# Kernel optimization log

Measured on AMD Instinct MI355X. Metric: run time of the kernel, lower is better.

Reference implementation:

```python
import jax, jax.numpy as jnp
import numpy as np
from jax import lax

# Fixed-point format: Q*.8 (8 fractional bits), as used by HGRNFixed8bit's
# to_fixed/from_fixed round-trip. We simulate it in float via round(x*256)/256.
FRAC = 256.0
EPS = 1e-5
B, T, D = 4, 2048, 2048  # batch, seq_len, hidden_size; input_dim = D (expand_ratio=1)


def to_fixed(x):
    return jnp.round(x * FRAC) / FRAC


def to_ternary(w):
    # BitNet-style ternarization: sign(w/mean|w|), zeroed where |w_norm| < 0.5
    scale = jnp.mean(jnp.abs(w))
    wn = w / (scale + 1e-5)
    t = jnp.sign(wn)
    return jnp.where(jnp.abs(wn) < 0.5, 0.0, t).astype(jnp.float32)


def per_channel_scale(w):
    # compute_scale: mean |w| over dim 0, stored in fixed point
    return to_fixed(jnp.mean(jnp.abs(w), axis=0))


def setup_inputs() -> dict:
    key = jax.random.key(0)
    ks = jax.random.split(key, 6)
    hidden_states = jax.random.normal(ks[0], (B, T, D), dtype=jnp.float32)
    # float master weights, then quantize exactly as quantize_weights() does
    w_i_f = jax.random.normal(ks[1], (D, D), dtype=jnp.float32) * 0.02  # i_proj.weight.T
    w_f_f = jax.random.normal(ks[2], (D, D), dtype=jnp.float32) * 0.02  # f_proj.weight.T
    w_g_f = jax.random.normal(ks[3], (D, D), dtype=jnp.float32) * 0.02  # g_proj.weight.T
    w_o_f = jax.random.normal(ks[4], (D, D), dtype=jnp.float32) * 0.02  # o_proj.weight [D_out, D_in]
    g_norm_w = jnp.ones((D,), dtype=jnp.float32)  # g_norm (RMSNorm-swish-gate) weight
    return {
        "hidden_states": hidden_states,
        "w_i": to_ternary(w_i_f), "w_f": to_ternary(w_f_f),
        "w_g": to_ternary(w_g_f), "w_o": to_ternary(w_o_f),
        "s_i": per_channel_scale(w_i_f), "s_f": per_channel_scale(w_f_f),
        "s_g": per_channel_scale(w_g_f), "s_o": per_channel_scale(w_o_f),
        "g_norm_w": g_norm_w,
    }


def reference(hidden_states, w_i, w_f, w_g, w_o, s_i, s_f, s_g, s_o, g_norm_w):
    # Quantize activations to 8-bit fixed point (to_fixed)
    x = to_fixed(hidden_states)                       # [B,T,D]
    # Ternary dequant-matmuls with per-channel scales
    i = jnp.einsum('btd,de->bte', x, w_i) * s_i       # input branch
    f = jax.nn.sigmoid(jnp.einsum('btd,de->bte', x, w_f) * s_f)  # forget gate
    g = jnp.einsum('btd,de->bte', x, w_g) * s_g       # output gate
    i = (1.0 - f) * i                                 # HGRN input gating
    # Gated linear recurrence h_t = f_t * h_{t-1} + i_t via associative scan
    def combine(a, b):
        af, ai = a
        bf, bi = b
        return (af * bf, ai * bf + bi)
    _, h = lax.associative_scan(combine, (f, i), axis=1)  # [B,T,E]
    # FusedRMSNormSwishGate: rmsnorm(h) * weight * swish(g)
    rms = h * lax.rsqrt(jnp.mean(h * h, axis=-1, keepdims=True) + EPS)
    o = rms * g_norm_w * (g * jax.nn.sigmoid(g))
    # Output ternary matmul (o_proj, weight untransposed -> use w_o.T),
    # per-input-channel scale, then from_fixed round-trip of the fixed output
    out = to_fixed(jnp.einsum('bte,oe->bto', o * s_o, w_o))  # [B,T,D]
    return out
```

## Files before the change

kernel.cpp:

```cpp
#include <hip/hip_runtime.h>
#include <hip/hip_bf16.h>
#include <stdint.h>
#include <math.h>


#define BATCH 4
#define SEQ   2048
#define DIM   2048
#define MROWS (BATCH*SEQ)
#define TCH   64
#define NCH   (SEQ/TCH)

#define BM 128
#define BN 128
#define BK 32

typedef unsigned short u16;
typedef __attribute__((ext_vector_type(8))) short short8;
typedef __attribute__((ext_vector_type(4))) float f32x4;

static __device__ __forceinline__ u16 f2bf_rne(float x) {
  uint32_t u = __float_as_uint(x);
  u += 0x7FFFu + ((u >> 16) & 1u);
  return (u16)(u >> 16);
}
static __device__ __forceinline__ float bf2f(u16 h) {
  return __uint_as_float(((uint32_t)h) << 16);
}

static __device__ __forceinline__ void gl2lds16(const void* g, void* l) {
  __builtin_amdgcn_global_load_lds((const __attribute__((address_space(1))) void*)g,
                                   (__attribute__((address_space(3))) void*)l,
                                   16, 0, 0);
}

__global__ __launch_bounds__(256) void diag_ws(float* __restrict__ out, float val) {
  size_t i = ((size_t)blockIdx.x * 256 + threadIdx.x) * 8;
#pragma unroll
  for (int j = 0; j < 8; j++) out[i + j] = val;
}

__global__ __launch_bounds__(256) void prep_x(const float* __restrict__ x,
                                              u16* __restrict__ XB) {
  size_t i = ((size_t)blockIdx.x * 256 + threadIdx.x) * 4;
  float4 v = *(const float4*)(x + i);
  float q[4] = {v.x, v.y, v.z, v.w};
  u16 hh[4];
#pragma unroll
  for (int j = 0; j < 4; j++) {
    float xq = rintf(q[j] * 256.0f) * 0.00390625f;
    hh[j] = f2bf_rne(xq);
  }
  *(uint2*)(XB + i) = make_uint2((uint32_t)hh[0] | ((uint32_t)hh[1] << 16),
                                 (uint32_t)hh[2] | ((uint32_t)hh[3] << 16));
}

__global__ void prep_wT(const float* __restrict__ w_i, const float* __restrict__ w_f,
                        const float* __restrict__ w_g, u16* __restrict__ WT) {
  __shared__ u16 tile[32][33];
  const int g = blockIdx.z;
  const float* __restrict__ w = (g == 0) ? w_i : (g == 1) ? w_f : w_g;
  u16* __restrict__ outp = WT + (size_t)g * DIM * DIM;
  const int d0 = blockIdx.x * 32;
  const int e0 = blockIdx.y * 32;
  const int tx = threadIdx.x;
  const int ty = threadIdx.y;
  for (int ii = ty; ii < 32; ii += 8)
    tile[ii][tx] = f2bf_rne(w[(size_t)(d0 + ii) * DIM + e0 + tx]);
  __syncthreads();
  for (int ii = ty; ii < 32; ii += 8)
    outp[(size_t)(e0 + ii) * DIM + d0 + tx] = tile[tx][ii];
}

__global__ __launch_bounds__(256) void prep_wo(const float* __restrict__ w, u16* __restrict__ WB) {
  size_t i = ((size_t)blockIdx.x * 256 + threadIdx.x) * 4;
  float4 v = *(const float4*)(w + i);
  *(uint2*)(WB + i) = make_uint2((uint32_t)f2bf_rne(v.x) | ((uint32_t)f2bf_rne(v.y) << 16),
                                 (uint32_t)f2bf_rne(v.z) | ((uint32_t)f2bf_rne(v.w) << 16));
}

__global__ __launch_bounds__(256) void gemm_gates(
    const u16* __restrict__ XB, const u16* __restrict__ WT,
    const float* __restrict__ s_i, const float* __restrict__ s_f, const float* __restrict__ s_g,
    const float* __restrict__ gnw, const float* __restrict__ s_o,
    u16* __restrict__ Ib, u16* __restrict__ Fb, u16* __restrict__ Gb) {
  __shared__ u16 sA[BM * BK];
  __shared__ u16 sB[BN * BK];

  const int bid = blockIdx.x;
  const int xcd = bid & 7;
  const int i5 = bid >> 3;
  const int gate = i5 >> 7;
  const int r = i5 & 127;
  const int n0 = (r & 15) * BN;
  const int m0 = (xcd * 8 + (r >> 4)) * BM;

  const u16* __restrict__ Wg = WT + (size_t)gate * DIM * DIM;
  const int tid = threadIdx.x;
  const int lane16 = tid & 15;
  const int quad = (tid & 63) >> 4;
  const int waveM = (tid >> 6) >> 1;
  const int waveN = (tid >> 6) & 1;
  const int srow = tid >> 2;
  const int scol = (tid & 3) * 8;

  f32x4 acc[4][4];
#pragma unroll
  for (int a = 0; a < 4; a++)
#pragma unroll
    for (int b = 0; b < 4; b++) acc[a][b] = {0.f, 0.f, 0.f, 0.f};

  for (int k0 = 0; k0 < DIM; k0 += BK) {
    __syncthreads();
#pragma unroll
    for (int j = 0; j < 2; j++) {
      const int row = srow + j * 64;
      gl2lds16(XB + (size_t)(m0 + row) * DIM + k0 + scol, sA + row * BK + scol);
      gl2lds16(Wg + (size_t)(n0 + row) * DIM + k0 + scol, sB + row * BK + scol);
    }
    __syncthreads();

    short8 af[4], bf[4];
#pragma unroll
    for (int mi = 0; mi < 4; mi++)
      af[mi] = *(const short8*)(sA + (waveM * 64 + mi * 16 + lane16) * BK + quad * 8);
#pragma unroll
    for (int ni = 0; ni < 4; ni++)
      bf[ni] = *(const short8*)(sB + (waveN * 64 + ni * 16 + lane16) * BK + quad * 8);
#pragma unroll
    for (int mi = 0; mi < 4; mi++)
#pragma unroll
      for (int ni = 0; ni < 4; ni++)
        acc[mi][ni] = __builtin_amdgcn_mfma_f32_16x16x32_bf16(af[mi], bf[ni], acc[mi][ni], 0, 0, 0);
  }

  const float* __restrict__ sc = (gate == 0) ? s_i : (gate == 1) ? s_f : s_g;
  u16* __restrict__ Out = (gate == 0) ? Ib : (gate == 1) ? Fb : Gb;
#pragma unroll
  for (int ni = 0; ni < 4; ni++) {
    const int n = n0 + waveN * 64 + ni * 16 + lane16;
    const float scale = sc[n];
    const float post = (gate == 2) ? gnw[n] * s_o[n] : 0.f;
#pragma unroll
    for (int mi = 0; mi < 4; mi++) {
      const int mbase = m0 + waveM * 64 + mi * 16 + quad * 4;
#pragma unroll
      for (int r2 = 0; r2 < 4; r2++) {
        float v = acc[mi][ni][r2] * scale;
        if (gate == 1) v = 1.0f / (1.0f + expf(-v));
        if (gate == 2) v = v / (1.0f + expf(-v)) * post;
        Out[(size_t)(mbase + r2) * DIM + n] = f2bf_rne(v);
      }
    }
  }
}

__global__ __launch_bounds__(256) void scan_phase1(const u16* __restrict__ Fb,
                                                   const u16* __restrict__ Ib,
                                                   float* __restrict__ Pc,
                                                   float* __restrict__ Sc) {
  const int e0 = (blockIdx.x * 256 + threadIdx.x) * 2;
  const int c = blockIdx.y;
  const int b = blockIdx.z;
  const size_t base = ((size_t)b * SEQ + (size_t)c * TCH) * DIM + e0;
  float P0 = 1.f, S0 = 0.f, P1 = 1.f, S1 = 0.f;
  for (int t = 0; t < TCH; t++) {
    const uint32_t fp = *(const uint32_t*)(Fb + base + (size_t)t * DIM);
    const uint32_t ip = *(const uint32_t*)(Ib + base + (size_t)t * DIM);
    const float f0 = bf2f((u16)fp), f1 = bf2f((u16)(fp >> 16));
    const float i0 = bf2f((u16)ip), i1 = bf2f((u16)(ip >> 16));
    S0 = S0 * f0 + (1.f - f0) * i0;  P0 *= f0;
    S1 = S1 * f1 + (1.f - f1) * i1;  P1 *= f1;
  }
  const size_t ci = ((size_t)b * NCH + c) * DIM + e0;
  *(float2*)(Pc + ci) = make_float2(P0, P1);
  *(float2*)(Sc + ci) = make_float2(S0, S1);
}

__global__ __launch_bounds__(256) void scan_phase2(const u16* __restrict__ Fb,
                                                   const u16* __restrict__ Ib,
                                                   const float* __restrict__ Pc,
                                                   const float* __restrict__ Sc,
                                                   u16* __restrict__ Hb) {
  const int e0 = (blockIdx.x * 256 + threadIdx.x) * 2;
  const int c = blockIdx.y;
  const int b = blockIdx.z;
  float h0 = 0.f, h1 = 0.f;
  for (int cc = 0; cc < c; cc++) {
    const size_t ci = ((size_t)b * NCH + cc) * DIM + e0;
    const float2 p = *(const float2*)(Pc + ci);
    const float2 s = *(const float2*)(Sc + ci);
    h0 = s.x + p.x * h0;
    h1 = s.y + p.y * h1;
  }
  const size_t base = ((size_t)b * SEQ + (size_t)c * TCH) * DIM + e0;
  for (int t = 0; t < TCH; t++) {
    const uint32_t fp = *(const uint32_t*)(Fb + base + (size_t)t * DIM);
    const uint32_t ip = *(const uint32_t*)(Ib + base + (size_t)t * DIM);
    const float f0 = bf2f((u16)fp), f1 = bf2f((u16)(fp >> 16));
    const float i0 = bf2f((u16)ip), i1 = bf2f((u16)(ip >> 16));
    h0 = f0 * h0 + (1.f - f0) * i0;
    h1 = f1 * h1 + (1.f - f1) * i1;
    *(uint32_t*)(Hb + base + (size_t)t * DIM) =
        (uint32_t)f2bf_rne(h0) | ((uint32_t)f2bf_rne(h1) << 16);
  }
}

__global__ __launch_bounds__(256) void rms_gate(const u16* __restrict__ Hb,
                                                const u16* __restrict__ SwGb,
                                                u16* __restrict__ OS) {
  const size_t base = (size_t)blockIdx.x * DIM;
  const int tid = threadIdx.x;
  const int e0 = tid * 8;
  uint4 hp = *(const uint4*)(Hb + base + e0);
  float hv[8];
  hv[0] = bf2f((u16)hp.x); hv[1] = bf2f((u16)(hp.x >> 16));
  hv[2] = bf2f((u16)hp.y); hv[3] = bf2f((u16)(hp.y >> 16));
  hv[4] = bf2f((u16)hp.z); hv[5] = bf2f((u16)(hp.z >> 16));
  hv[6] = bf2f((u16)hp.w); hv[7] = bf2f((u16)(hp.w >> 16));
  float ss = 0.f;
#pragma unroll
  for (int j = 0; j < 8; j++) ss += hv[j] * hv[j];
#pragma unroll
  for (int off = 32; off > 0; off >>= 1) ss += __shfl_down(ss, off, 64);
  __shared__ float red[4];
  if ((tid & 63) == 0) red[tid >> 6] = ss;
  __syncthreads();
  const float tot = red[0] + red[1] + red[2] + red[3];
  const float inv = 1.0f / sqrtf(tot * (1.0f / (float)DIM) + 1e-5f);

  uint4 gp = *(const uint4*)(SwGb + base + e0);
  float gv[8];
  gv[0] = bf2f((u16)gp.x); gv[1] = bf2f((u16)(gp.x >> 16));
  gv[2] = bf2f((u16)gp.y); gv[3] = bf2f((u16)(gp.y >> 16));
  gv[4] = bf2f((u16)gp.z); gv[5] = bf2f((u16)(gp.z >> 16));
  gv[6] = bf2f((u16)gp.w); gv[7] = bf2f((u16)(gp.w >> 16));
  u16 ov[8];
#pragma unroll
  for (int j = 0; j < 8; j++) ov[j] = f2bf_rne(hv[j] * inv * gv[j]);
  uint4 op;
  op.x = (uint32_t)ov[0] | ((uint32_t)ov[1] << 16);
  op.y = (uint32_t)ov[2] | ((uint32_t)ov[3] << 16);
  op.z = (uint32_t)ov[4] | ((uint32_t)ov[5] << 16);
  op.w = (uint32_t)ov[6] | ((uint32_t)ov[7] << 16);
  *(uint4*)(OS + base + e0) = op;
}

__global__ __launch_bounds__(256) void gemm_out(const u16* __restrict__ OS,
                                                const u16* __restrict__ WOB,
                                                float* __restrict__ out) {
  __shared__ u16 sA[BM * BK];
  __shared__ u16 sB[BN * BK];

  const int bid = blockIdx.x;
  const int xcd = bid & 7;
  const int i5 = bid >> 3;
  const int n0 = (i5 & 15) * BN;
  const int m0 = (xcd * 8 + (i5 >> 4)) * BM;

  const int tid = threadIdx.x;
  const int lane16 = tid & 15;
  const int quad = (tid & 63) >> 4;
  const int waveM = (tid >> 6) >> 1;
  const int waveN = (tid >> 6) & 1;
  const int srow = tid >> 2;
  const int scol = (tid & 3) * 8;

  f32x4 acc[4][4];
#pragma unroll
  for (int a = 0; a < 4; a++)
#pragma unroll
    for (int b = 0; b < 4; b++) acc[a][b] = {0.f, 0.f, 0.f, 0.f};

  for (int k0 = 0; k0 < DIM; k0 += BK) {
    __syncthreads();
#pragma unroll
    for (int j = 0; j < 2; j++) {
      const int row = srow + j * 64;
      gl2lds16(OS + (size_t)(m0 + row) * DIM + k0 + scol, sA + row * BK + scol);
      gl2lds16(WOB + (size_t)(n0 + row) * DIM + k0 + scol, sB + row * BK + scol);
    }
    __syncthreads();

    short8 af[4], bf[4];
#pragma unroll
    for (int mi = 0; mi < 4; mi++)
      af[mi] = *(const short8*)(sA + (waveM * 64 + mi * 16 + lane16) * BK + quad * 8);
#pragma unroll
    for (int ni = 0; ni < 4; ni++)
      bf[ni] = *(const short8*)(sB + (waveN * 64 + ni * 16 + lane16) * BK + quad * 8);
#pragma unroll
    for (int mi = 0; mi < 4; mi++)
#pragma unroll
      for (int ni = 0; ni < 4; ni++)
        acc[mi][ni] = __builtin_amdgcn_mfma_f32_16x16x32_bf16(af[mi], bf[ni], acc[mi][ni], 0, 0, 0);
  }

#pragma unroll
  for (int ni = 0; ni < 4; ni++) {
    const int n = n0 + waveN * 64 + ni * 16 + lane16;
#pragma unroll
    for (int mi = 0; mi < 4; mi++) {
      const int mbase = m0 + waveM * 64 + mi * 16 + quad * 4;
#pragma unroll
      for (int r2 = 0; r2 < 4; r2++) {
        const float v = acc[mi][ni][r2];
        out[(size_t)(mbase + r2) * DIM + n] = rintf(v * 256.0f) * 0.00390625f;
      }
    }
  }
}

extern "C" void kernel_launch(void* const* d_in, const int* in_sizes, int n_in,
                              void* d_out, int out_size, void* d_ws, size_t ws_size,
                              hipStream_t stream) {
  (void)in_sizes; (void)n_in; (void)out_size;
  const float* x   = (const float*)d_in[0];
  const float* w_i = (const float*)d_in[1];
  const float* w_f = (const float*)d_in[2];
  const float* w_g = (const float*)d_in[3];
  const float* w_o = (const float*)d_in[4];
  const float* s_i = (const float*)d_in[5];
  const float* s_f = (const float*)d_in[6];
  const float* s_g = (const float*)d_in[7];
  const float* s_o = (const float*)d_in[8];
  const float* gnw = (const float*)d_in[9];
  float* out = (float*)d_out;

  const size_t MB = 1024 * 1024;
  const size_t NEED = 88 * MB;
  if (ws_size < NEED) {
    diag_ws<<<MROWS * DIM / 2048, 256, 0, stream>>>(out, (float)(ws_size / MB));
    return;
  }

  uint8_t* ws = (uint8_t*)d_ws;
  u16* XB = (u16*)(ws);
  u16* WT = (u16*)(ws + 32 * MB);
  u16* Ib = (u16*)(ws + 56 * MB);
  float* Pc = (float*)(ws + 32 * MB);
  float* Sc = (float*)(ws + 33 * MB);
  u16* WOB = (u16*)(ws + 34 * MB);
  u16* Hb  = XB;
  u16* OS  = Ib;
  u16* Gb = (u16*)d_out;
  u16* Fb = (u16*)((uint8_t*)d_out + 32 * MB);

  prep_x<<<MROWS * DIM / 1024, 256, 0, stream>>>(x, XB);
  prep_wT<<<dim3(DIM / 32, DIM / 32, 3), dim3(32, 8, 1), 0, stream>>>(w_i, w_f, w_g, WT);
  gemm_gates<<<3072, 256, 0, stream>>>(XB, WT, s_i, s_f, s_g, gnw, s_o, Ib, Fb, Gb);
  scan_phase1<<<dim3(DIM / 512, NCH, BATCH), 256, 0, stream>>>(Fb, Ib, Pc, Sc);
  scan_phase2<<<dim3(DIM / 512, NCH, BATCH), 256, 0, stream>>>(Fb, Ib, Pc, Sc, Hb);
  prep_wo<<<DIM * DIM / 1024, 256, 0, stream>>>(w_o, WOB);
  rms_gate<<<MROWS, 256, 0, stream>>>(Hb, Gb, OS);
  gemm_out<<<1024, 256, 0, stream>>>(OS, WOB, out);
}
```

Baseline: 570.8 us.

## Rewrite both GEMMs with 256x128x64 tiles, triple-buffered LDS pipeline and swizzle

Both bf16 GEMMs are replaced by a shared k-loop that uses 512-thread blocks, 256x128 tiles with BK=64, and a three-stage LDS ring. The A and B prefetches for tile t+2 are interleaved between the MFMA halves, with s_setprio and explicit vmcnt waits. The LDS layout is XOR-swizzled to avoid bank conflicts. Epilogues stage results through LDS so global stores are coalesced 16-byte writes. This aims to hide global latency and raise MFMA utilization, at the cost of more LDS per block (about 144KB, so likely one block per CU despite the launch bound) and more complex synchronization.

```diff
diff --git a/kernel.cpp b/kernel.cpp
--- a/kernel.cpp
+++ b/kernel.cpp
@@ -11,9 +11,13 @@
 #define TCH   64
 #define NCH   (SEQ/TCH)
 
-#define BM 128
-#define BN 128
-#define BK 32
+#define GBM 256
+#define GBN 128
+#define GBK 64
+#define GNT (DIM/GBK)
+#define ASZ (GBM*GBK)
+#define BSZ (GBN*GBK)
+#define BUFSZ (ASZ+BSZ)
 
 typedef unsigned short u16;
 typedef __attribute__((ext_vector_type(8))) short short8;
@@ -79,79 +83,209 @@
                                  (uint32_t)f2bf_rne(v.z) | ((uint32_t)f2bf_rne(v.w) << 16));
 }
 
-__global__ __launch_bounds__(256) void gemm_gates(
+static __device__ __forceinline__ void stage_A(const u16* ga, u16* buf, int tid) {
+#pragma unroll
+  for (int j = 0; j < 4; j++)
+    gl2lds16(ga + (size_t)j * (64 * DIM), buf + (size_t)(tid + j * 512) * 8);
+}
+static __device__ __forceinline__ void stage_B(const u16* gb, u16* buf, int tid) {
+#pragma unroll
+  for (int j = 0; j < 2; j++)
+    gl2lds16(gb + (size_t)j * (64 * DIM), buf + ASZ + (size_t)(tid + j * 512) * 8);
+}
+
+static __device__ __forceinline__ void kloop(const u16* __restrict__ Ag,
+                                             const u16* __restrict__ Bg,
+                                             u16* lds, f32x4 (&acc)[4][4]) {
+  const int tid = threadIdx.x;
+  const int lane16 = tid & 15;
+  const int quad = (tid & 63) >> 4;
+  const int wid = tid >> 6;
+  const int waveM = wid >> 1;
+  const int waveN = wid & 1;
+  const int rowA = tid >> 3;
+  const int cc8 = ((tid & 7) ^ (rowA & 7)) * 8;
+  const u16* ga = Ag + (size_t)rowA * DIM + cc8;
+  const u16* gb = Bg + (size_t)rowA * DIM + cc8;
+  const int colx = (lane16 & 7) * 8;
+  const int arow = (waveM * 64 + lane16) * GBK;
+  const int brow = (waveN * 64 + lane16) * GBK;
+
+  stage_A(ga, lds, tid);
+  stage_B(gb, lds, tid);
+  stage_A(ga + GBK, lds + BUFSZ, tid);
+  stage_B(gb + GBK, lds + BUFSZ, tid);
+  asm volatile("s_waitcnt vmcnt(6)" ::: "memory");
+  __builtin_amdgcn_s_barrier();
+
+  int sl = 0, st = 2;
+#pragma unroll 1
+  for (int t = 0; t < GNT; ++t) {
+    const u16* A = lds + sl * BUFSZ;
+    const u16* B = A + ASZ;
+    u16* SB = lds + st * BUFSZ;
+    const bool pf = (t + 2 < GNT);
+    {
+      short8 af[4], bf[4];
+      const int c0 = (quad * 8) ^ colx;
+#pragma unroll
+      for (int mi = 0; mi < 4; mi++)
+        af[mi] = *(const short8*)(A + arow + mi * (16 * GBK) + c0);
+#pragma unroll
+      for (int ni = 0; ni < 4; ni++)
+        bf[ni] = *(const short8*)(B + brow + ni * (16 * GBK) + c0);
+      if (pf) stage_A(ga + (size_t)(t + 2) * GBK, SB, tid);
+      __builtin_amdgcn_s_barrier();
+      __builtin_amdgcn_s_setprio(1);
+#pragma unroll
+      for (int mi = 0; mi < 4; mi++)
+#pragma unroll
+        for (int ni = 0; ni < 4; ni++)
+          acc[mi][ni] = __builtin_amdgcn_mfma_f32_16x16x32_bf16(af[mi], bf[ni], acc[mi][ni], 0, 0, 0);
+      __builtin_amdgcn_s_setprio(0);
+      __builtin_amdgcn_s_barrier();
+    }
+    {
+      short8 af[4], bf[4];
+      const int c1 = (32 + quad * 8) ^ colx;
+#pragma unroll
+      for (int mi = 0; mi < 4; mi++)
+        af[mi] = *(const short8*)(A + arow + mi * (16 * GBK) + c1);
+#pragma unroll
+      for (int ni = 0; ni < 4; ni++)
+        bf[ni] = *(const short8*)(B + brow + ni * (16 * GBK) + c1);
+      if (pf) stage_B(gb + (size_t)(t + 2) * GBK, SB, tid);
+      __builtin_amdgcn_s_barrier();
+      __builtin_amdgcn_s_setprio(1);
+#pragma unroll
+      for (int mi = 0; mi < 4; mi++)
+#pragma unroll
+        for (int ni = 0; ni < 4; ni++)
+          acc[mi][ni] = __builtin_amdgcn_mfma_f32_16x16x32_bf16(af[mi], bf[ni], acc[mi][ni], 0, 0, 0);
+      __builtin_amdgcn_s_setprio(0);
+      __builtin_amdgcn_s_barrier();
+    }
+    if (pf) {
+      asm volatile("s_waitcnt vmcnt(6)" ::: "memory");
+    } else if (t + 1 < GNT) {
+      asm volatile("s_waitcnt vmcnt(0)" ::: "memory");
+    }
+    __builtin_amdgcn_s_barrier();
+    sl = (sl == 2) ? 0 : sl + 1;
+    st = (st == 2) ? 0 : st + 1;
+  }
+}
+
+__global__ __launch_bounds__(512, 2) void gemm_gates8(
     const u16* __restrict__ XB, const u16* __restrict__ WT,
     const float* __restrict__ s_i, const float* __restrict__ s_f, const float* __restrict__ s_g,
     const float* __restrict__ gnw, const float* __restrict__ s_o,
     u16* __restrict__ Ib, u16* __restrict__ Fb, u16* __restrict__ Gb) {
-  __shared__ u16 sA[BM * BK];
-  __shared__ u16 sB[BN * BK];
-
+  __shared__ __align__(16) u16 lds[3 * BUFSZ];
   const int bid = blockIdx.x;
-  const int xcd = bid & 7;
-  const int i5 = bid >> 3;
-  const int gate = i5 >> 7;
-  const int r = i5 & 127;
-  const int n0 = (r & 15) * BN;
-  const int m0 = (xcd * 8 + (r >> 4)) * BM;
-
-  const u16* __restrict__ Wg = WT + (size_t)gate * DIM * DIM;
+  const int i = (bid & 7) * 192 + (bid >> 3);
+  const int gate = i >> 9;
+  const int r = i & 511;
+  const int m0 = (r >> 4) * GBM;
+  const int n0 = (r & 15) * GBN;
+
+  const u16* Ag = XB + (size_t)m0 * DIM;
+  const u16* Bg = WT + (size_t)gate * DIM * DIM + (size_t)n0 * DIM;
+
+  f32x4 acc[4][4];
+#pragma unroll
+  for (int a = 0; a < 4; a++)
+#pragma unroll
+    for (int b = 0; b < 4; b++) acc[a][b] = {0.f, 0.f, 0.f, 0.f};
+
+  kloop(Ag, Bg, lds, acc);
+
+  __syncthreads();
   const int tid = threadIdx.x;
   const int lane16 = tid & 15;
   const int quad = (tid & 63) >> 4;
-  const int waveM = (tid >> 6) >> 1;
-  const int waveN = (tid >> 6) & 1;
-  const int srow = tid >> 2;
-  const int scol = (tid & 3) * 8;
-
-  f32x4 acc[4][4];
-#pragma unroll
-  for (int a = 0; a < 4; a++)
-#pragma unroll
-    for (int b = 0; b < 4; b++) acc[a][b] = {0.f, 0.f, 0.f, 0.f};
-
-  for (int k0 = 0; k0 < DIM; k0 += BK) {
-    __syncthreads();
-#pragma unroll
-    for (int j = 0; j < 2; j++) {
-      const int row = srow + j * 64;
-      gl2lds16(XB + (size_t)(m0 + row) * DIM + k0 + scol, sA + row * BK + scol);
-      gl2lds16(Wg + (size_t)(n0 + row) * DIM + k0 + scol, sB + row * BK + scol);
-    }
-    __syncthreads();
-
-    short8 af[4], bf[4];
-#pragma unroll
-    for (int mi = 0; mi < 4; mi++)
-      af[mi] = *(const short8*)(sA + (waveM * 64 + mi * 16 + lane16) * BK + quad * 8);
-#pragma unroll
-    for (int ni = 0; ni < 4; ni++)
-      bf[ni] = *(const short8*)(sB + (waveN * 64 + ni * 16 + lane16) * BK + quad * 8);
-#pragma unroll
-    for (int mi = 0; mi < 4; mi++)
-#pragma unroll
-      for (int ni = 0; ni < 4; ni++)
-        acc[mi][ni] = __builtin_amdgcn_mfma_f32_16x16x32_bf16(af[mi], bf[ni], acc[mi][ni], 0, 0, 0);
-  }
-
+  const int wid = tid >> 6;
+  const int waveM = wid >> 1;
+  const int waveN = wid & 1;
   const float* __restrict__ sc = (gate == 0) ? s_i : (gate == 1) ? s_f : s_g;
-  u16* __restrict__ Out = (gate == 0) ? Ib : (gate == 1) ? Fb : Gb;
+  u16* T = lds;
 #pragma unroll
   for (int ni = 0; ni < 4; ni++) {
     const int n = n0 + waveN * 64 + ni * 16 + lane16;
     const float scale = sc[n];
     const float post = (gate == 2) ? gnw[n] * s_o[n] : 0.f;
+    const int tcol = waveN * 64 + ni * 16 + lane16;
 #pragma unroll
     for (int mi = 0; mi < 4; mi++) {
-      const int mbase = m0 + waveM * 64 + mi * 16 + quad * 4;
+      const int lrow = waveM * 64 + mi * 16 + quad * 4;
 #pragma unroll
       for (int r2 = 0; r2 < 4; r2++) {
         float v = acc[mi][ni][r2] * scale;
         if (gate == 1) v = 1.0f / (1.0f + expf(-v));
         if (gate == 2) v = v / (1.0f + expf(-v)) * post;
-        Out[(size_t)(mbase + r2) * DIM + n] = f2bf_rne(v);
+        T[(lrow + r2) * 136 + tcol] = f2bf_rne(v);
       }
     }
+  }
+  __syncthreads();
+  u16* __restrict__ Out = (gate == 0) ? Ib : (gate == 1) ? Fb : Gb;
+#pragma unroll
+  for (int j = 0; j < 8; j++) {
+    const int id = tid + j * 512;
+    const int row = id >> 4;
+    const int c16 = id & 15;
+    uint4 v = *(const uint4*)(T + row * 136 + c16 * 8);
+    *(uint4*)(Out + (size_t)(m0 + row) * DIM + n0 + c16 * 8) = v;
+  }
+}
+
+__global__ __launch_bounds__(512, 2) void gemm_out8(const u16* __restrict__ OS,
+                                                    const u16* __restrict__ WOB,
+                                                    float* __restrict__ out) {
+  __shared__ __align__(16) u16 lds[3 * BUFSZ];
+  const int bid = blockIdx.x;
+  const int i = (bid & 7) * 64 + (bid >> 3);
+  const int m0 = (i >> 4) * GBM;
+  const int n0 = (i & 15) * GBN;
+
+  const u16* Ag = OS + (size_t)m0 * DIM;
+  const u16* Bg = WOB + (size_t)n0 * DIM;
+
+  f32x4 acc[4][4];
+#pragma unroll
+  for (int a = 0; a < 4; a++)
+#pragma unroll
+    for (int b = 0; b < 4; b++) acc[a][b] = {0.f, 0.f, 0.f, 0.f};
+
+  kloop(Ag, Bg, lds, acc);
+
+  __syncthreads();
+  const int tid = threadIdx.x;
+  const int lane16 = tid & 15;
+  const int quad = (tid & 63) >> 4;
+  const int wid = tid >> 6;
+  const int waveM = wid >> 1;
+  const int waveN = wid & 1;
+  float* T = (float*)lds;
+#pragma unroll
+  for (int ni = 0; ni < 4; ni++) {
+    const int tcol = waveN * 64 + ni * 16 + lane16;
+#pragma unroll
+    for (int mi = 0; mi < 4; mi++) {
+      const int lrow = waveM * 64 + mi * 16 + quad * 4;
+#pragma unroll
+      for (int r2 = 0; r2 < 4; r2++)
+        T[(lrow + r2) * 132 + tcol] = rintf(acc[mi][ni][r2] * 256.0f) * 0.00390625f;
+    }
+  }
+  __syncthreads();
+#pragma unroll
+  for (int j = 0; j < 16; j++) {
+    const int id = tid + j * 512;
+    const int row = id >> 5;
+    const int c4 = id & 31;
+    float4 v = *(const float4*)(T + row * 132 + c4 * 4);
+    *(float4*)(out + (size_t)(m0 + row) * DIM + n0 + c4 * 4) = v;
   }
 }
 
@@ -246,71 +380,6 @@
   *(uint4*)(OS + base + e0) = op;
 }
 
-__global__ __launch_bounds__(256) void gemm_out(const u16* __restrict__ OS,
-                                                const u16* __restrict__ WOB,
-                                                float* __restrict__ out) {
-  __shared__ u16 sA[BM * BK];
-  __shared__ u16 sB[BN * BK];
-
-  const int bid = blockIdx.x;
-  const int xcd = bid & 7;
-  const int i5 = bid >> 3;
-  const int n0 = (i5 & 15) * BN;
-  const int m0 = (xcd * 8 + (i5 >> 4)) * BM;
-
-  const int tid = threadIdx.x;
-  const int lane16 = tid & 15;
-  const int quad = (tid & 63) >> 4;
-  const int waveM = (tid >> 6) >> 1;
-  const int waveN = (tid >> 6) & 1;
-  const int srow = tid >> 2;
-  const int scol = (tid & 3) * 8;
-
-  f32x4 acc[4][4];
-#pragma unroll
-  for (int a = 0; a < 4; a++)
-#pragma unroll
-    for (int b = 0; b < 4; b++) acc[a][b] = {0.f, 0.f, 0.f, 0.f};
-
-  for (int k0 = 0; k0 < DIM; k0 += BK) {
-    __syncthreads();
-#pragma unroll
-    for (int j = 0; j < 2; j++) {
-      const int row = srow + j * 64;
-      gl2lds16(OS + (size_t)(m0 + row) * DIM + k0 + scol, sA + row * BK + scol);
-      gl2lds16(WOB + (size_t)(n0 + row) * DIM + k0 + scol, sB + row * BK + scol);
-    }
-    __syncthreads();
-
-    short8 af[4], bf[4];
-#pragma unroll
-    for (int mi = 0; mi < 4; mi++)
-      af[mi] = *(const short8*)(sA + (waveM * 64 + mi * 16 + lane16) * BK + quad * 8);
-#pragma unroll
-    for (int ni = 0; ni < 4; ni++)
-      bf[ni] = *(const short8*)(sB + (waveN * 64 + ni * 16 + lane16) * BK + quad * 8);
-#pragma unroll
-    for (int mi = 0; mi < 4; mi++)
-#pragma unroll
-      for (int ni = 0; ni < 4; ni++)
-        acc[mi][ni] = __builtin_amdgcn_mfma_f32_16x16x32_bf16(af[mi], bf[ni], acc[mi][ni], 0, 0, 0);
-  }
-
-#pragma unroll
-  for (int ni = 0; ni < 4; ni++) {
-    const int n = n0 + waveN * 64 + ni * 16 + lane16;
-#pragma unroll
-    for (int mi = 0; mi < 4; mi++) {
-      const int mbase = m0 + waveM * 64 + mi * 16 + quad * 4;
-#pragma unroll
-      for (int r2 = 0; r2 < 4; r2++) {
-        const float v = acc[mi][ni][r2];
-        out[(size_t)(mbase + r2) * DIM + n] = rintf(v * 256.0f) * 0.00390625f;
-      }
-    }
-  }
-}
-
 extern "C" void kernel_launch(void* const* d_in, const int* in_sizes, int n_in,
                               void* d_out, int out_size, void* d_ws, size_t ws_size,
                               hipStream_t stream) {
@@ -348,10 +417,10 @@
 
   prep_x<<<MROWS * DIM / 1024, 256, 0, stream>>>(x, XB);
   prep_wT<<<dim3(DIM / 32, DIM / 32, 3), dim3(32, 8, 1), 0, stream>>>(w_i, w_f, w_g, WT);
-  gemm_gates<<<3072, 256, 0, stream>>>(XB, WT, s_i, s_f, s_g, gnw, s_o, Ib, Fb, Gb);
+  gemm_gates8<<<1536, 512, 0, stream>>>(XB, WT, s_i, s_f, s_g, gnw, s_o, Ib, Fb, Gb);
   scan_phase1<<<dim3(DIM / 512, NCH, BATCH), 256, 0, stream>>>(Fb, Ib, Pc, Sc);
   scan_phase2<<<dim3(DIM / 512, NCH, BATCH), 256, 0, stream>>>(Fb, Ib, Pc, Sc, Hb);
   prep_wo<<<DIM * DIM / 1024, 256, 0, stream>>>(w_o, WOB);
   rms_gate<<<MROWS, 256, 0, stream>>>(Hb, Gb, OS);
-  gemm_out<<<1024, 256, 0, stream>>>(OS, WOB, out);
-}
+  gemm_out8<<<512, 512, 0, stream>>>(OS, WOB, out);
+}
```

Measured after the change: 551.3 us. 1.04x faster.
